# Performance work log

Hardware: AMD Instinct MI355X
Metric: run time of the kernel (lower is better)

The kernel has to match this reference:

```python
import jax, jax.numpy as jnp
import numpy as np
import math

B, S, D, H, PD = 2, 2048, 1024, 16, 3
DK = D // H          # 64
SP = S // H          # 128, required so physics_scores matches scores shape


def setup_inputs() -> dict:
    key = jax.random.key(0)
    ks = jax.random.split(key, 16)
    sc = 0.02
    return {
        "query": jax.random.normal(ks[0], (B, S, D), jnp.float32),
        "key_in": jax.random.normal(ks[1], (B, S, D), jnp.float32),
        "value": jax.random.normal(ks[2], (B, S, D), jnp.float32),
        "physics_info": jax.random.normal(ks[3], (B, SP, PD), jnp.float32),
        "Wq": jax.random.normal(ks[4], (D, D), jnp.float32) * sc,
        "bq": jnp.zeros((D,), jnp.float32),
        "Wk": jax.random.normal(ks[5], (D, D), jnp.float32) * sc,
        "bk": jnp.zeros((D,), jnp.float32),
        "Wv": jax.random.normal(ks[6], (D, D), jnp.float32) * sc,
        "bv": jnp.zeros((D,), jnp.float32),
        "Wo": jax.random.normal(ks[7], (D, D), jnp.float32) * sc,
        "bo": jnp.zeros((D,), jnp.float32),
        "Pw": jax.random.normal(ks[8], (PD, D), jnp.float32),   # physics_weight
        "pb": jnp.zeros((1,), jnp.float32),                      # physics_bias
    }


def reference(query, key_in, value, physics_info, Wq, bq, Wk, bk, Wv, bv, Wo, bo, Pw, pb):
    b, s, d = query.shape
    inv = 1.0 / math.sqrt(DK)
    # project and split heads -> [B, H, S, DK]
    Q = (query @ Wq + bq).reshape(b, s, H, DK).transpose(0, 2, 1, 3)
    K = (key_in @ Wk + bk).reshape(b, s, H, DK).transpose(0, 2, 1, 3)
    V = (value @ Wv + bv).reshape(b, s, H, DK).transpose(0, 2, 1, 3)
    scores = jnp.einsum('bhqd,bhkd->bhqk', Q, K) * inv  # [B,H,S,S]
    # physics constraint: [B,SP,D] -> (expand over heads is a no-op) -> [B,SP*H,DK]
    pc = (physics_info @ Pw).reshape(b, SP * H, DK)
    physics_scores = jnp.einsum('bhqd,bkd->bhqk', Q, pc) * inv  # [B,H,S,S]
    scores = scores + pb[0] * physics_scores
    attn = jax.nn.softmax(scores, axis=-1)  # dropout in eval mode (identity)
    ctx = jnp.einsum('bhqk,bhkd->bhqd', attn, V)
    ctx = ctx.transpose(0, 2, 1, 3).reshape(b, s, d)
    return ctx @ Wo + bo
```

## Files before the change

### kernel.cpp

```cpp
#include <hip/hip_runtime.h>
#include <hip/hip_bf16.h>
#include <stdint.h>
#include <math.h>

typedef __bf16 bf16_t;
typedef __attribute__((ext_vector_type(8))) __bf16 bf16x8;
typedef __attribute__((ext_vector_type(4))) __bf16 bf16x4;
typedef __attribute__((ext_vector_type(4))) short short4_t;
typedef __attribute__((ext_vector_type(4))) float f32x4;

#define GLOBAL_AS(p) ((const __attribute__((address_space(1))) void*)(p))
#define LDS_AS(p)    ((__attribute__((address_space(3))) void*)(p))

#define B_ 2
#define S_ 2048
#define D_ 1024
#define H_ 16
#define DK_ 64
#define SP_ 128

#define QSCALE 0.1803368801111144f

static __device__ inline float fast_exp2(float x) {
#if __has_builtin(__builtin_amdgcn_exp2f)
    return __builtin_amdgcn_exp2f(x);
#else
    return __expf(x * 0.6931471805599453f);
#endif
}

static __device__ inline f32x4 mfma16x16x16bf16(short4_t a, short4_t b, f32x4 c) {
#if __has_builtin(__builtin_amdgcn_mfma_f32_16x16x16bf16_1k)
    return __builtin_amdgcn_mfma_f32_16x16x16bf16_1k(a, b, c, 0, 0, 0);
#else
    asm volatile("v_mfma_f32_16x16x16_bf16 %0, %1, %2, %0" : "+v"(c) : "v"(a), "v"(b));
    return c;
#endif
}

struct WPtrs { const float* w[4]; bf16_t* o[4]; };

__global__ __launch_bounds__(256) void prep(
    const float* __restrict__ q, const float* __restrict__ k,
    const float* __restrict__ v,
    bf16_t* __restrict__ qo, bf16_t* __restrict__ ko, bf16_t* __restrict__ vo,
    WPtrs wp, const float* __restrict__ phys, const float* __restrict__ Pw,
    float* __restrict__ PP) {
    int bx = blockIdx.x, tid = threadIdx.x;
    if (bx < 6144) {
        int z = bx >> 11, blk = bx & 2047;
        const float* in = (z == 0) ? q : (z == 1) ? k : v;
        bf16_t* out = (z == 0) ? qo : (z == 1) ? ko : vo;
        size_t i = ((size_t)blk * 256 + tid) * 8;
        f32x4 a = *(const f32x4*)(in + i);
        f32x4 b = *(const f32x4*)(in + i + 4);
        bf16x8 o;
#pragma unroll
        for (int e = 0; e < 4; ++e) { o[e] = (bf16_t)a[e]; o[4 + e] = (bf16_t)b[e]; }
        *(bf16x8*)(out + i) = o;
    } else if (bx < 10240) {
        __shared__ bf16_t t[32][33];
        int idx = bx - 6144;
        int z = idx >> 10;
        const float* W = wp.w[z];
        bf16_t* Wt = wp.o[z];
        int gx = (idx & 31) * 32, gy = ((idx >> 5) & 31) * 32;
        int x = tid & 31, y0 = tid >> 5;
#pragma unroll
        for (int j = 0; j < 32; j += 8)
            t[y0 + j][x] = (bf16_t)W[(size_t)(gy + y0 + j) * D_ + gx + x];
        __syncthreads();
#pragma unroll
        for (int j = 0; j < 32; j += 8)
            Wt[(size_t)(gx + y0 + j) * D_ + gy + x] = t[x][y0 + j];
    } else {
        int i = (bx - 10240) * 256 + tid;
        int n = i & (D_ - 1);
        int sb = i >> 10;
        float acc = 0.f;
#pragma unroll
        for (int p = 0; p < 3; ++p)
            acc += phys[sb * 3 + p] * Pw[p * D_ + n];
        PP[i] = acc;
    }
}

#define TSTR 272

__global__ __launch_bounds__(256) void qkv_gemm(
    const bf16_t* __restrict__ Qi, const bf16_t* __restrict__ Ki,
    const bf16_t* __restrict__ Vi,
    const bf16_t* __restrict__ WqT, const bf16_t* __restrict__ WkT,
    const bf16_t* __restrict__ WvT,
    const float* __restrict__ bq, const float* __restrict__ bk,
    const float* __restrict__ bv,
    bf16_t* __restrict__ Qo, bf16_t* __restrict__ Ko, bf16_t* __restrict__ Vo,
    const float* __restrict__ PP, const float* __restrict__ pbp) {
    __shared__ alignas(16) char smem[40960];
    bf16_t* lA = (bf16_t*)smem;
    bf16_t* lB = (bf16_t*)(smem + 16384);
    int z = blockIdx.z;
    const bf16_t* A = (z == 0) ? Qi : (z == 1) ? Ki : Vi;
    const bf16_t* Bt = (z == 0) ? WqT : (z == 1) ? WkT : WvT;
    const float* bias = (z == 0) ? bq : (z == 1) ? bk : bv;

    int tid = threadIdx.x;
    int lane = tid & 63, wid = tid >> 6;
    int quad = lane >> 4, l15 = lane & 15;
    int bm = blockIdx.x * 128;
    int bn = blockIdx.y * 128;
    int wm = (wid >> 1) * 64, wn = (wid & 1) * 64;
    f32x4 acc[4][4] = {};

    for (int k0 = 0; k0 < D_; k0 += 64) {
        __syncthreads();
        const char* gA = (const char*)(A + (size_t)bm * D_ + k0);
        const char* gB = (const char*)(Bt + (size_t)bn * D_ + k0);
#pragma unroll
        for (int j = 0; j < 4; ++j) {
            int woff = j * 4096 + wid * 1024;
            int fl = woff + lane * 16;
            int row = fl >> 7, col = fl & 127;
            __builtin_amdgcn_global_load_lds(GLOBAL_AS(gA + (size_t)row * (D_ * 2) + col),
                                             LDS_AS((char*)lA + woff), 16, 0, 0);
            __builtin_amdgcn_global_load_lds(GLOBAL_AS(gB + (size_t)row * (D_ * 2) + col),
                                             LDS_AS((char*)lB + woff), 16, 0, 0);
        }
        __syncthreads();
#pragma unroll
        for (int ks = 0; ks < 2; ++ks) {
            bf16x8 af[4], bfr[4];
#pragma unroll
            for (int i = 0; i < 4; ++i) {
                af[i] = *(const bf16x8*)((const char*)lA + (wm + i * 16 + l15) * 128 + ks * 64 + quad * 16);
                bfr[i] = *(const bf16x8*)((const char*)lB + (wn + i * 16 + l15) * 128 + ks * 64 + quad * 16);
            }
#pragma unroll
            for (int i = 0; i < 4; ++i)
#pragma unroll
                for (int j = 0; j < 4; ++j)
                    acc[i][j] = __builtin_amdgcn_mfma_f32_16x16x32_bf16(af[i], bfr[j], acc[i][j], 0, 0, 0);
        }
    }

    __syncthreads();
    float pb0 = (z == 1) ? pbp[0] : 0.f;
    char* T = smem;
#pragma unroll
    for (int i = 0; i < 4; ++i)
#pragma unroll
        for (int j = 0; j < 4; ++j) {
            int rl0 = wm + i * 16 + quad * 4;
            int c = wn + j * 16 + l15;
            float bv_ = bias[bn + c];
            if (z == 2) {
                bf16x4 t4;
#pragma unroll
                for (int reg = 0; reg < 4; ++reg) t4[reg] = (bf16_t)(acc[i][j][reg] + bv_);
                *(bf16x4*)(T + c * TSTR + rl0 * 2) = t4;
            } else if (z == 1) {
#pragma unroll
                for (int reg = 0; reg < 4; ++reg) {
                    int r = bm + rl0 + reg;
                    int b = r >> 11, s = r & (S_ - 1);
                    float v = acc[i][j][reg] + bv_ +
                              pb0 * PP[((size_t)(b * SP_ + (s >> 4)) << 10) + ((s & 15) << 6) + ((bn + c) & 63)];
                    *(bf16_t*)(T + (rl0 + reg) * TSTR + c * 2) = (bf16_t)v;
                }
            } else {
#pragma unroll
                for (int reg = 0; reg < 4; ++reg)
                    *(bf16_t*)(T + (rl0 + reg) * TSTR + c * 2) = (bf16_t)((acc[i][j][reg] + bv_) * QSCALE);
            }
        }
    __syncthreads();
    if (z == 2) {
        int b = bm >> 11, s0 = bm & (S_ - 1);
        char* gout = (char*)Vo + (((size_t)(b << 10) + bn) * S_ + s0) * 2;
#pragma unroll
        for (int it = 0; it < 8; ++it) {
            int chunk = it * 256 + tid;
            int row = chunk >> 4, c16 = chunk & 15;
            bf16x8 v = *(const bf16x8*)(T + row * TSTR + c16 * 16);
            *(bf16x8*)(gout + (size_t)row * (S_ * 2) + c16 * 16) = v;
        }
    } else {
        bf16_t* O = (z == 0) ? Qo : Ko;
        char* gout = (char*)(O + (size_t)bm * D_ + bn);
#pragma unroll
        for (int it = 0; it < 8; ++it) {
            int chunk = it * 256 + tid;
            int row = chunk >> 4, c16 = chunk & 15;
            bf16x8 v = *(const bf16x8*)(T + row * TSTR + c16 * 16);
            *(bf16x8*)(gout + (size_t)row * (D_ * 2) + c16 * 16) = v;
        }
    }
}

#define KSTR 144
#define VSTR 272

__global__ __launch_bounds__(256) void flash_attn(const bf16_t* Qb,
                                                  const bf16_t* __restrict__ Kb,
                                                  const bf16_t* __restrict__ Vt,
                                                  bf16_t* Ctx) {
    __shared__ alignas(16) char lK[128 * KSTR];
    __shared__ alignas(16) char lV[64 * VSTR];
    int tid = threadIdx.x, lane = tid & 63, wid = tid >> 6;
    int quad = lane >> 4, l15 = lane & 15;
    int q0 = blockIdx.x * 128;
    int h = blockIdx.y, b = blockIdx.z;
    const bf16_t* Qh = Qb + ((size_t)b * S_) * D_ + h * DK_;
    const bf16_t* Kh = Kb + ((size_t)b * S_) * D_ + h * DK_;
    const bf16_t* Vh = Vt + ((size_t)b * D_ + h * DK_) * S_;

    {
        const char* g = (const char*)(Qh + (size_t)q0 * D_);
#pragma unroll
        for (int j = 0; j < 4; ++j) {
            int flat = j * 4096 + tid * 16;
            bf16x8 v = *(const bf16x8*)(g + (size_t)(flat >> 7) * (D_ * 2) + (flat & 127));
            *(bf16x8*)(lK + (flat >> 7) * KSTR + (flat & 127)) = v;
        }
    }
    __syncthreads();
    bf16x8 qf[2][2];
#pragma unroll
    for (int mt = 0; mt < 2; ++mt)
#pragma unroll
        for (int ks = 0; ks < 2; ++ks)
            qf[mt][ks] = *(const bf16x8*)(lK + (wid * 32 + mt * 16 + l15) * KSTR + ks * 64 + quad * 16);

    f32x4 ot[4][2] = {};
    float l_i[2] = {0.f, 0.f};

    for (int t = 0; t < S_ / 128; ++t) {
        const char* gK = (const char*)(Kh + (size_t)t * 128 * D_);
        const char* gV = (const char*)(Vh + (size_t)t * 128);
        bf16x8 vk[4], vv[4];
#pragma unroll
        for (int j = 0; j < 4; ++j) {
            int flat = j * 4096 + tid * 16;
            vk[j] = *(const bf16x8*)(gK + (size_t)(flat >> 7) * (D_ * 2) + (flat & 127));
            vv[j] = *(const bf16x8*)(gV + (size_t)(flat >> 8) * (S_ * 2) + (flat & 255));
        }
        __syncthreads();
#pragma unroll
        for (int j = 0; j < 4; ++j) {
            int flat = j * 4096 + tid * 16;
            *(bf16x8*)(lK + (flat >> 7) * KSTR + (flat & 127)) = vk[j];
            *(bf16x8*)(lV + (flat >> 8) * VSTR + (flat & 255)) = vv[j];
        }
        __syncthreads();

        f32x4 sc[8][2];
#pragma unroll
        for (int kt = 0; kt < 8; ++kt)
#pragma unroll
            for (int mt = 0; mt < 2; ++mt) sc[kt][mt] = (f32x4){0.f, 0.f, 0.f, 0.f};
#pragma unroll
        for (int kt = 0; kt < 8; ++kt) {
            bf16x8 kf0 = *(const bf16x8*)(lK + (kt * 16 + l15) * KSTR + quad * 16);
            bf16x8 kf1 = *(const bf16x8*)(lK + (kt * 16 + l15) * KSTR + 64 + quad * 16);
#pragma unroll
            for (int mt = 0; mt < 2; ++mt) {
                sc[kt][mt] = __builtin_amdgcn_mfma_f32_16x16x32_bf16(kf0, qf[mt][0], sc[kt][mt], 0, 0, 0);
                sc[kt][mt] = __builtin_amdgcn_mfma_f32_16x16x32_bf16(kf1, qf[mt][1], sc[kt][mt], 0, 0, 0);
            }
        }

#pragma unroll
        for (int mt = 0; mt < 2; ++mt) {
            float rsum = 0.f;
#pragma unroll
            for (int kt = 0; kt < 8; ++kt)
#pragma unroll
                for (int r = 0; r < 4; ++r) {
                    float p = fast_exp2(sc[kt][mt][r]);
                    sc[kt][mt][r] = p;
                    rsum += p;
                }
            rsum += __shfl_xor(rsum, 16, 64);
            rsum += __shfl_xor(rsum, 32, 64);
            l_i[mt] += rsum;
        }

#pragma unroll
        for (int kt = 0; kt < 8; ++kt) {
            short4_t bp[2];
#pragma unroll
            for (int mt = 0; mt < 2; ++mt) {
                bf16x4 t4;
#pragma unroll
                for (int r = 0; r < 4; ++r) t4[r] = (bf16_t)sc[kt][mt][r];
                bp[mt] = *(short4_t*)&t4;
            }
#pragma unroll
            for (int dt = 0; dt < 4; ++dt) {
                bf16x4 a4 = *(const bf16x4*)(lV + (dt * 16 + l15) * VSTR + kt * 32 + quad * 8);
                short4_t ap = *(short4_t*)&a4;
#pragma unroll
                for (int mt = 0; mt < 2; ++mt)
                    ot[dt][mt] = mfma16x16x16bf16(ap, bp[mt], ot[dt][mt]);
            }
        }
    }

    __syncthreads();
#pragma unroll
    for (int mt = 0; mt < 2; ++mt) {
        float inv_l = 1.0f / l_i[mt];
#pragma unroll
        for (int dt = 0; dt < 4; ++dt) {
            bf16x4 t4;
#pragma unroll
            for (int r = 0; r < 4; ++r) t4[r] = (bf16_t)(ot[dt][mt][r] * inv_l);
            *(bf16x4*)(lK + (wid * 32 + mt * 16 + l15) * KSTR + dt * 32 + quad * 8) = t4;
        }
    }
    __syncthreads();
    {
        char* gout = (char*)(Ctx + ((size_t)b * S_ + q0) * D_ + h * DK_);
#pragma unroll
        for (int j = 0; j < 4; ++j) {
            int flat = j * 4096 + tid * 16;
            bf16x8 v = *(const bf16x8*)(lK + (flat >> 7) * KSTR + (flat & 127));
            *(bf16x8*)(gout + (size_t)(flat >> 7) * (D_ * 2) + (flat & 127)) = v;
        }
    }
}

__global__ __launch_bounds__(256) void gemm_out(const bf16_t* __restrict__ A,
                                                const bf16_t* __restrict__ Bt,
                                                const float* __restrict__ bias,
                                                float* __restrict__ C) {
    __shared__ alignas(16) bf16_t lA[128 * 64];
    __shared__ alignas(16) bf16_t lB[128 * 64];
    int tid = threadIdx.x;
    int lane = tid & 63, wid = tid >> 6;
    int quad = lane >> 4, l15 = lane & 15;
    int bm = blockIdx.x * 128;
    int bn = blockIdx.y * 128;
    int wm = (wid >> 1) * 64, wn = (wid & 1) * 64;
    f32x4 acc[4][4] = {};

    for (int k0 = 0; k0 < D_; k0 += 64) {
        __syncthreads();
        const char* gA = (const char*)(A + (size_t)bm * D_ + k0);
        const char* gB = (const char*)(Bt + (size_t)bn * D_ + k0);
#pragma unroll
        for (int j = 0; j < 4; ++j) {
            int woff = j * 4096 + wid * 1024;
            int fl = woff + lane * 16;
            int row = fl >> 7, col = fl & 127;
            __builtin_amdgcn_global_load_lds(GLOBAL_AS(gA + (size_t)row * (D_ * 2) + col),
                                             LDS_AS((char*)lA + woff), 16, 0, 0);
            __builtin_amdgcn_global_load_lds(GLOBAL_AS(gB + (size_t)row * (D_ * 2) + col),
                                             LDS_AS((char*)lB + woff), 16, 0, 0);
        }
        __syncthreads();
#pragma unroll
        for (int ks = 0; ks < 2; ++ks) {
            bf16x8 af[4], bfr[4];
#pragma unroll
            for (int i = 0; i < 4; ++i) {
                af[i] = *(const bf16x8*)((const char*)lA + (wm + i * 16 + l15) * 128 + ks * 64 + quad * 16);
                bfr[i] = *(const bf16x8*)((const char*)lB + (wn + i * 16 + l15) * 128 + ks * 64 + quad * 16);
            }
#pragma unroll
            for (int i = 0; i < 4; ++i)
#pragma unroll
                for (int j = 0; j < 4; ++j)
                    acc[i][j] = __builtin_amdgcn_mfma_f32_16x16x32_bf16(af[i], bfr[j], acc[i][j], 0, 0, 0);
        }
    }
#pragma unroll
    for (int i = 0; i < 4; ++i)
#pragma unroll
        for (int j = 0; j < 4; ++j) {
            int r0 = bm + wm + i * 16 + quad * 4;
            int c = bn + wn + j * 16 + l15;
            float bv_ = bias[c];
#pragma unroll
            for (int reg = 0; reg < 4; ++reg)
                C[(size_t)(r0 + reg) * D_ + c] = acc[i][j][reg] + bv_;
        }
}

extern "C" void kernel_launch(void* const* d_in, const int* in_sizes, int n_in,
                              void* d_out, int out_size, void* d_ws, size_t ws_size,
                              hipStream_t stream) {
    const float* query  = (const float*)d_in[0];
    const float* key_in = (const float*)d_in[1];
    const float* value  = (const float*)d_in[2];
    const float* phys   = (const float*)d_in[3];
    const float* Wq     = (const float*)d_in[4];
    const float* bq     = (const float*)d_in[5];
    const float* Wk     = (const float*)d_in[6];
    const float* bk     = (const float*)d_in[7];
    const float* Wv     = (const float*)d_in[8];
    const float* bv     = (const float*)d_in[9];
    const float* Wo     = (const float*)d_in[10];
    const float* bo     = (const float*)d_in[11];
    const float* Pw     = (const float*)d_in[12];
    const float* pb     = (const float*)d_in[13];

    char* ws = (char*)d_ws;
    const size_t MB = 1ull << 20;
    bf16_t* Kb  = (bf16_t*)(ws + 0 * MB);
    bf16_t* QC  = (bf16_t*)(ws + 8 * MB);
    bf16_t* Kin = (bf16_t*)(ws + 16 * MB);
    bf16_t* Vin = (bf16_t*)(ws + 24 * MB);
    bf16_t* WqT = (bf16_t*)(ws + 32 * MB);
    bf16_t* WkT = (bf16_t*)(ws + 34 * MB);
    bf16_t* WvT = (bf16_t*)(ws + 36 * MB);
    bf16_t* WoT = (bf16_t*)(ws + 38 * MB);
    float*  PP  = (float*)(ws + 40 * MB);
    bf16_t* Vt  = (bf16_t*)d_out;
    bf16_t* Qin = (bf16_t*)((char*)d_out + 8 * MB);

    WPtrs wp;
    wp.w[0] = Wq; wp.w[1] = Wk; wp.w[2] = Wv; wp.w[3] = Wo;
    wp.o[0] = WqT; wp.o[1] = WkT; wp.o[2] = WvT; wp.o[3] = WoT;

    prep<<<11264, 256, 0, stream>>>(query, key_in, value, Qin, Kin, Vin,
                                    wp, phys, Pw, PP);

    dim3 gq(32, 8, 3);
    qkv_gemm<<<gq, 256, 0, stream>>>(Qin, Kin, Vin, WqT, WkT, WvT,
                                     bq, bk, bv, QC, Kb, Vt, PP, pb);

    dim3 fg(S_ / 128, H_, B_);
    flash_attn<<<fg, 256, 0, stream>>>(QC, Kb, Vt, QC);

    dim3 gg(32, 8);
    gemm_out<<<gg, 256, 0, stream>>>(QC, WoT, bo, (float*)d_out);
}
```

Baseline: 249.2 us.

## Double-buffer flash attention K/V via direct-to-LDS loads with XOR swizzle

Rewrites the attention kernel's K/V staging to use global_load_lds into double-buffered LDS tiles. The next tile's load is issued before computing on the current one, so memory latency overlaps MFMA work. Padded LDS strides are replaced with XOR-swizzled layouts to avoid bank conflicts. The grid is remapped to a 1D launch so heads sharing K/V land on the same XCD, and s_setprio is raised around the MFMA sections. The costs are 64KB of LDS per block, which lowers occupancy, and more complex manual waitcnt and barrier handling.

New measurement: 263.4 us. 5.7% more time.

```diff
diff --git a/kernel.cpp b/kernel.cpp
--- a/kernel.cpp
+++ b/kernel.cpp
@@ -197,19 +197,21 @@
     }
 }
 
-#define KSTR 144
-#define VSTR 272
-
 __global__ __launch_bounds__(256) void flash_attn(const bf16_t* Qb,
                                                   const bf16_t* __restrict__ Kb,
                                                   const bf16_t* __restrict__ Vt,
                                                   bf16_t* Ctx) {
-    __shared__ alignas(16) char lK[128 * KSTR];
-    __shared__ alignas(16) char lV[64 * VSTR];
+    __shared__ alignas(16) char lds[65536];
     int tid = threadIdx.x, lane = tid & 63, wid = tid >> 6;
     int quad = lane >> 4, l15 = lane & 15;
-    int q0 = blockIdx.x * 128;
-    int h = blockIdx.y, b = blockIdx.z;
+    int r7 = l15 & 7;
+
+    int bid = blockIdx.x;
+    int xcd = bid & 7, slot = bid >> 3;
+    int yz = xcd * 4 + (slot >> 4);
+    int q0 = (slot & 15) * 128;
+    int h = yz & 15, b = yz >> 4;
+
     const bf16_t* Qh = Qb + ((size_t)b * S_) * D_ + h * DK_;
     const bf16_t* Kh = Kb + ((size_t)b * S_) * D_ + h * DK_;
     const bf16_t* Vh = Vt + ((size_t)b * D_ + h * DK_) * S_;
@@ -219,8 +221,9 @@
 #pragma unroll
         for (int j = 0; j < 4; ++j) {
             int flat = j * 4096 + tid * 16;
-            bf16x8 v = *(const bf16x8*)(g + (size_t)(flat >> 7) * (D_ * 2) + (flat & 127));
-            *(bf16x8*)(lK + (flat >> 7) * KSTR + (flat & 127)) = v;
+            int row = flat >> 7, ch = (flat >> 4) & 7;
+            bf16x8 v = *(const bf16x8*)(g + (size_t)row * (D_ * 2) + (ch << 4));
+            *(bf16x8*)(lds + row * 128 + ((ch ^ (row & 7)) << 4)) = v;
         }
     }
     __syncthreads();
@@ -229,45 +232,69 @@
     for (int mt = 0; mt < 2; ++mt)
 #pragma unroll
         for (int ks = 0; ks < 2; ++ks)
-            qf[mt][ks] = *(const bf16x8*)(lK + (wid * 32 + mt * 16 + l15) * KSTR + ks * 64 + quad * 16);
+            qf[mt][ks] = *(const bf16x8*)(lds + (wid * 32 + mt * 16 + l15) * 128 +
+                                          ((((ks << 2) | quad) ^ r7) << 4));
+    asm volatile("s_waitcnt lgkmcnt(0)" ::: "memory");
+    __builtin_amdgcn_sched_barrier(0);
+    __builtin_amdgcn_s_barrier();
+
+    auto STAGE = [&](int t) {
+        char* bK = lds + (t & 1) * 16384;
+        char* bV = lds + 32768 + (t & 1) * 16384;
+        const char* gK = (const char*)(Kh + (size_t)t * 128 * D_);
+        const char* gV = (const char*)(Vh + (size_t)t * 128);
+#pragma unroll
+        for (int j = 0; j < 4; ++j) {
+            int flat = j * 4096 + tid * 16;
+            int row = flat >> 7, ch = (flat >> 4) & 7;
+            __builtin_amdgcn_global_load_lds(
+                GLOBAL_AS(gK + (size_t)row * (D_ * 2) + ((ch ^ (row & 7)) << 4)),
+                LDS_AS(bK + flat), 16, 0, 0);
+        }
+#pragma unroll
+        for (int j = 0; j < 4; ++j) {
+            int flat = j * 4096 + tid * 16;
+            int row = flat >> 8, ch = (flat >> 4) & 15;
+            __builtin_amdgcn_global_load_lds(
+                GLOBAL_AS(gV + (size_t)row * (S_ * 2) + ((ch ^ (row & 15)) << 4)),
+                LDS_AS(bV + flat), 16, 0, 0);
+        }
+    };
 
     f32x4 ot[4][2] = {};
     float l_i[2] = {0.f, 0.f};
 
+    STAGE(0);
+
     for (int t = 0; t < S_ / 128; ++t) {
-        const char* gK = (const char*)(Kh + (size_t)t * 128 * D_);
-        const char* gV = (const char*)(Vh + (size_t)t * 128);
-        bf16x8 vk[4], vv[4];
-#pragma unroll
-        for (int j = 0; j < 4; ++j) {
-            int flat = j * 4096 + tid * 16;
-            vk[j] = *(const bf16x8*)(gK + (size_t)(flat >> 7) * (D_ * 2) + (flat & 127));
-            vv[j] = *(const bf16x8*)(gV + (size_t)(flat >> 8) * (S_ * 2) + (flat & 255));
-        }
-        __syncthreads();
-#pragma unroll
-        for (int j = 0; j < 4; ++j) {
-            int flat = j * 4096 + tid * 16;
-            *(bf16x8*)(lK + (flat >> 7) * KSTR + (flat & 127)) = vk[j];
-            *(bf16x8*)(lV + (flat >> 8) * VSTR + (flat & 255)) = vv[j];
-        }
-        __syncthreads();
+        asm volatile("s_waitcnt vmcnt(0)" ::: "memory");
+        __builtin_amdgcn_s_barrier();
+        __builtin_amdgcn_sched_barrier(0);
+
+        if (t < S_ / 128 - 1) STAGE(t + 1);
+        __builtin_amdgcn_sched_barrier(0);
+
+        const char* bK = lds + (t & 1) * 16384;
+        const char* bV = lds + 32768 + (t & 1) * 16384;
 
         f32x4 sc[8][2];
 #pragma unroll
         for (int kt = 0; kt < 8; ++kt)
 #pragma unroll
             for (int mt = 0; mt < 2; ++mt) sc[kt][mt] = (f32x4){0.f, 0.f, 0.f, 0.f};
+        __builtin_amdgcn_s_setprio(1);
 #pragma unroll
         for (int kt = 0; kt < 8; ++kt) {
-            bf16x8 kf0 = *(const bf16x8*)(lK + (kt * 16 + l15) * KSTR + quad * 16);
-            bf16x8 kf1 = *(const bf16x8*)(lK + (kt * 16 + l15) * KSTR + 64 + quad * 16);
+            int row = kt * 16 + l15;
+            bf16x8 kf0 = *(const bf16x8*)(bK + row * 128 + ((quad ^ r7) << 4));
+            bf16x8 kf1 = *(const bf16x8*)(bK + row * 128 + (((quad | 4) ^ r7) << 4));
 #pragma unroll
             for (int mt = 0; mt < 2; ++mt) {
                 sc[kt][mt] = __builtin_amdgcn_mfma_f32_16x16x32_bf16(kf0, qf[mt][0], sc[kt][mt], 0, 0, 0);
                 sc[kt][mt] = __builtin_amdgcn_mfma_f32_16x16x32_bf16(kf1, qf[mt][1], sc[kt][mt], 0, 0, 0);
             }
         }
+        __builtin_amdgcn_s_setprio(0);
 
 #pragma unroll
         for (int mt = 0; mt < 2; ++mt) {
@@ -285,6 +312,7 @@
             l_i[mt] += rsum;
         }
 
+        __builtin_amdgcn_s_setprio(1);
 #pragma unroll
         for (int kt = 0; kt < 8; ++kt) {
             short4_t bp[2];
@@ -297,25 +325,30 @@
             }
 #pragma unroll
             for (int dt = 0; dt < 4; ++dt) {
-                bf16x4 a4 = *(const bf16x4*)(lV + (dt * 16 + l15) * VSTR + kt * 32 + quad * 8);
+                int row = dt * 16 + l15;
+                int ch = (kt * 2 + (quad >> 1)) ^ l15;
+                bf16x4 a4 = *(const bf16x4*)(bV + row * 256 + (ch << 4) + ((quad & 1) << 3));
                 short4_t ap = *(short4_t*)&a4;
 #pragma unroll
                 for (int mt = 0; mt < 2; ++mt)
                     ot[dt][mt] = mfma16x16x16bf16(ap, bp[mt], ot[dt][mt]);
             }
         }
+        __builtin_amdgcn_s_setprio(0);
     }
 
     __syncthreads();
 #pragma unroll
     for (int mt = 0; mt < 2; ++mt) {
         float inv_l = 1.0f / l_i[mt];
+        int row = wid * 32 + mt * 16 + l15;
 #pragma unroll
         for (int dt = 0; dt < 4; ++dt) {
             bf16x4 t4;
 #pragma unroll
             for (int r = 0; r < 4; ++r) t4[r] = (bf16_t)(ot[dt][mt][r] * inv_l);
-            *(bf16x4*)(lK + (wid * 32 + mt * 16 + l15) * KSTR + dt * 32 + quad * 8) = t4;
+            int ch = (dt * 2 + (quad >> 1)) ^ r7;
+            *(bf16x4*)(lds + row * 128 + (ch << 4) + ((quad & 1) << 3)) = t4;
         }
     }
     __syncthreads();
@@ -324,8 +357,9 @@
 #pragma unroll
         for (int j = 0; j < 4; ++j) {
             int flat = j * 4096 + tid * 16;
-            bf16x8 v = *(const bf16x8*)(lK + (flat >> 7) * KSTR + (flat & 127));
-            *(bf16x8*)(gout + (size_t)(flat >> 7) * (D_ * 2) + (flat & 127)) = v;
+            int row = flat >> 7, ch = (flat >> 4) & 7;
+            bf16x8 v = *(const bf16x8*)(lds + row * 128 + ((ch ^ (row & 7)) << 4));
+            *(bf16x8*)(gout + (size_t)row * (D_ * 2) + (ch << 4)) = v;
         }
     }
 }
@@ -430,8 +464,7 @@
     qkv_gemm<<<gq, 256, 0, stream>>>(Qin, Kin, Vin, WqT, WkT, WvT,
                                      bq, bk, bv, QC, Kb, Vt, PP, pb);
 
-    dim3 fg(S_ / 128, H_, B_);
-    flash_attn<<<fg, 256, 0, stream>>>(QC, Kb, Vt, QC);
+    flash_attn<<<512, 256, 0, stream>>>(QC, Kb, Vt, QC);
 
     dim3 gg(32, 8);
     gemm_out<<<gg, 256, 0, stream>>>(QC, WoT, bo, (float*)d_out);
```

## Restructure flash attention to 8 waves with prefetch, XCD-aware block mapping, setprio

Applied to the files above, without the earlier changes.

The flash attention kernel now runs 512 threads per block, so each wave owns 16 query rows instead of 32, which halves per-wave register state and allows more waves per CU. The next K/V tile is loaded into registers while the current tile is being computed, overlapping global loads with MFMA work. A 1D grid is remapped so that blocks landing on the same XCD share the same (batch, head) and reuse K/V in L2. s_setprio raises wave priority around the MFMA sections. The trade-offs are that each K/V tile in LDS is now amortized over fewer query rows per wave, and every block pays more barrier overhead.

Result: no change. 253.4 us (+1.7%).

```diff
diff --git a/kernel.cpp b/kernel.cpp
--- a/kernel.cpp
+++ b/kernel.cpp
@@ -200,16 +200,21 @@
 #define KSTR 144
 #define VSTR 272
 
-__global__ __launch_bounds__(256) void flash_attn(const bf16_t* Qb,
-                                                  const bf16_t* __restrict__ Kb,
-                                                  const bf16_t* __restrict__ Vt,
-                                                  bf16_t* Ctx) {
+__global__ __launch_bounds__(512, 4) void flash_attn(const bf16_t* Qb,
+                                                     const bf16_t* __restrict__ Kb,
+                                                     const bf16_t* __restrict__ Vt,
+                                                     bf16_t* Ctx) {
     __shared__ alignas(16) char lK[128 * KSTR];
     __shared__ alignas(16) char lV[64 * VSTR];
     int tid = threadIdx.x, lane = tid & 63, wid = tid >> 6;
     int quad = lane >> 4, l15 = lane & 15;
-    int q0 = blockIdx.x * 128;
-    int h = blockIdx.y, b = blockIdx.z;
+
+    int bid = blockIdx.x;
+    int xcd = bid & 7, slot = bid >> 3;
+    int yz = xcd * 4 + (slot >> 4);
+    int q0 = (slot & 15) * 128;
+    int h = yz & 15, b = yz >> 4;
+
     const bf16_t* Qh = Qb + ((size_t)b * S_) * D_ + h * DK_;
     const bf16_t* Kh = Kb + ((size_t)b * S_) * D_ + h * DK_;
     const bf16_t* Vh = Vt + ((size_t)b * D_ + h * DK_) * S_;
@@ -217,113 +222,113 @@
     {
         const char* g = (const char*)(Qh + (size_t)q0 * D_);
 #pragma unroll
-        for (int j = 0; j < 4; ++j) {
-            int flat = j * 4096 + tid * 16;
+        for (int j = 0; j < 2; ++j) {
+            int flat = j * 8192 + tid * 16;
             bf16x8 v = *(const bf16x8*)(g + (size_t)(flat >> 7) * (D_ * 2) + (flat & 127));
             *(bf16x8*)(lK + (flat >> 7) * KSTR + (flat & 127)) = v;
         }
     }
     __syncthreads();
-    bf16x8 qf[2][2];
-#pragma unroll
-    for (int mt = 0; mt < 2; ++mt)
-#pragma unroll
-        for (int ks = 0; ks < 2; ++ks)
-            qf[mt][ks] = *(const bf16x8*)(lK + (wid * 32 + mt * 16 + l15) * KSTR + ks * 64 + quad * 16);
-
-    f32x4 ot[4][2] = {};
-    float l_i[2] = {0.f, 0.f};
-
-    for (int t = 0; t < S_ / 128; ++t) {
-        const char* gK = (const char*)(Kh + (size_t)t * 128 * D_);
-        const char* gV = (const char*)(Vh + (size_t)t * 128);
-        bf16x8 vk[4], vv[4];
-#pragma unroll
-        for (int j = 0; j < 4; ++j) {
-            int flat = j * 4096 + tid * 16;
+    bf16x8 qf[2];
+#pragma unroll
+    for (int ks = 0; ks < 2; ++ks)
+        qf[ks] = *(const bf16x8*)(lK + (wid * 16 + l15) * KSTR + ks * 64 + quad * 16);
+    __syncthreads();
+
+    f32x4 ot[4] = {};
+    float l_i = 0.f;
+
+    bf16x8 vk[2], vv[2];
+    const int NT = S_ / 128;
+    {
+        const char* gK = (const char*)Kh;
+        const char* gV = (const char*)Vh;
+#pragma unroll
+        for (int j = 0; j < 2; ++j) {
+            int flat = j * 8192 + tid * 16;
             vk[j] = *(const bf16x8*)(gK + (size_t)(flat >> 7) * (D_ * 2) + (flat & 127));
             vv[j] = *(const bf16x8*)(gV + (size_t)(flat >> 8) * (S_ * 2) + (flat & 255));
         }
-        __syncthreads();
-#pragma unroll
-        for (int j = 0; j < 4; ++j) {
-            int flat = j * 4096 + tid * 16;
+    }
+
+    for (int t = 0; t < NT; ++t) {
+#pragma unroll
+        for (int j = 0; j < 2; ++j) {
+            int flat = j * 8192 + tid * 16;
             *(bf16x8*)(lK + (flat >> 7) * KSTR + (flat & 127)) = vk[j];
             *(bf16x8*)(lV + (flat >> 8) * VSTR + (flat & 255)) = vv[j];
         }
         __syncthreads();
 
-        f32x4 sc[8][2];
-#pragma unroll
-        for (int kt = 0; kt < 8; ++kt)
-#pragma unroll
-            for (int mt = 0; mt < 2; ++mt) sc[kt][mt] = (f32x4){0.f, 0.f, 0.f, 0.f};
+        if (t + 1 < NT) {
+            const char* gK = (const char*)(Kh + (size_t)(t + 1) * 128 * D_);
+            const char* gV = (const char*)(Vh + (size_t)(t + 1) * 128);
+#pragma unroll
+            for (int j = 0; j < 2; ++j) {
+                int flat = j * 8192 + tid * 16;
+                vk[j] = *(const bf16x8*)(gK + (size_t)(flat >> 7) * (D_ * 2) + (flat & 127));
+                vv[j] = *(const bf16x8*)(gV + (size_t)(flat >> 8) * (S_ * 2) + (flat & 255));
+            }
+        }
+
+        f32x4 sc[8];
+#pragma unroll
+        for (int kt = 0; kt < 8; ++kt) sc[kt] = (f32x4){0.f, 0.f, 0.f, 0.f};
+        __builtin_amdgcn_s_setprio(1);
 #pragma unroll
         for (int kt = 0; kt < 8; ++kt) {
             bf16x8 kf0 = *(const bf16x8*)(lK + (kt * 16 + l15) * KSTR + quad * 16);
             bf16x8 kf1 = *(const bf16x8*)(lK + (kt * 16 + l15) * KSTR + 64 + quad * 16);
-#pragma unroll
-            for (int mt = 0; mt < 2; ++mt) {
-                sc[kt][mt] = __builtin_amdgcn_mfma_f32_16x16x32_bf16(kf0, qf[mt][0], sc[kt][mt], 0, 0, 0);
-                sc[kt][mt] = __builtin_amdgcn_mfma_f32_16x16x32_bf16(kf1, qf[mt][1], sc[kt][mt], 0, 0, 0);
-            }
-        }
-
-#pragma unroll
-        for (int mt = 0; mt < 2; ++mt) {
-            float rsum = 0.f;
-#pragma unroll
-            for (int kt = 0; kt < 8; ++kt)
-#pragma unroll
-                for (int r = 0; r < 4; ++r) {
-                    float p = fast_exp2(sc[kt][mt][r]);
-                    sc[kt][mt][r] = p;
-                    rsum += p;
-                }
-            rsum += __shfl_xor(rsum, 16, 64);
-            rsum += __shfl_xor(rsum, 32, 64);
-            l_i[mt] += rsum;
-        }
-
+            sc[kt] = __builtin_amdgcn_mfma_f32_16x16x32_bf16(kf0, qf[0], sc[kt], 0, 0, 0);
+            sc[kt] = __builtin_amdgcn_mfma_f32_16x16x32_bf16(kf1, qf[1], sc[kt], 0, 0, 0);
+        }
+        __builtin_amdgcn_s_setprio(0);
+
+        float rsum = 0.f;
+#pragma unroll
+        for (int kt = 0; kt < 8; ++kt)
+#pragma unroll
+            for (int r = 0; r < 4; ++r) {
+                float p = fast_exp2(sc[kt][r]);
+                sc[kt][r] = p;
+                rsum += p;
+            }
+        rsum += __shfl_xor(rsum, 16, 64);
+        rsum += __shfl_xor(rsum, 32, 64);
+        l_i += rsum;
+
+        __builtin_amdgcn_s_setprio(1);
 #pragma unroll
         for (int kt = 0; kt < 8; ++kt) {
-            short4_t bp[2];
-#pragma unroll
-            for (int mt = 0; mt < 2; ++mt) {
-                bf16x4 t4;
-#pragma unroll
-                for (int r = 0; r < 4; ++r) t4[r] = (bf16_t)sc[kt][mt][r];
-                bp[mt] = *(short4_t*)&t4;
-            }
+            bf16x4 t4;
+#pragma unroll
+            for (int r = 0; r < 4; ++r) t4[r] = (bf16_t)sc[kt][r];
+            short4_t bp = *(short4_t*)&t4;
 #pragma unroll
             for (int dt = 0; dt < 4; ++dt) {
                 bf16x4 a4 = *(const bf16x4*)(lV + (dt * 16 + l15) * VSTR + kt * 32 + quad * 8);
                 short4_t ap = *(short4_t*)&a4;
-#pragma unroll
-                for (int mt = 0; mt < 2; ++mt)
-                    ot[dt][mt] = mfma16x16x16bf16(ap, bp[mt], ot[dt][mt]);
-            }
-        }
-    }
-
-    __syncthreads();
-#pragma unroll
-    for (int mt = 0; mt < 2; ++mt) {
-        float inv_l = 1.0f / l_i[mt];
-#pragma unroll
-        for (int dt = 0; dt < 4; ++dt) {
-            bf16x4 t4;
-#pragma unroll
-            for (int r = 0; r < 4; ++r) t4[r] = (bf16_t)(ot[dt][mt][r] * inv_l);
-            *(bf16x4*)(lK + (wid * 32 + mt * 16 + l15) * KSTR + dt * 32 + quad * 8) = t4;
-        }
+                ot[dt] = mfma16x16x16bf16(ap, bp, ot[dt]);
+            }
+        }
+        __builtin_amdgcn_s_setprio(0);
+        __syncthreads();
+    }
+
+    float inv_l = 1.0f / l_i;
+#pragma unroll
+    for (int dt = 0; dt < 4; ++dt) {
+        bf16x4 t4;
+#pragma unroll
+        for (int r = 0; r < 4; ++r) t4[r] = (bf16_t)(ot[dt][r] * inv_l);
+        *(bf16x4*)(lK + (wid * 16 + l15) * KSTR + dt * 32 + quad * 8) = t4;
     }
     __syncthreads();
     {
         char* gout = (char*)(Ctx + ((size_t)b * S_ + q0) * D_ + h * DK_);
 #pragma unroll
-        for (int j = 0; j < 4; ++j) {
-            int flat = j * 4096 + tid * 16;
+        for (int j = 0; j < 2; ++j) {
+            int flat = j * 8192 + tid * 16;
             bf16x8 v = *(const bf16x8*)(lK + (flat >> 7) * KSTR + (flat & 127));
             *(bf16x8*)(gout + (size_t)(flat >> 7) * (D_ * 2) + (flat & 127)) = v;
         }
@@ -430,8 +435,7 @@
     qkv_gemm<<<gq, 256, 0, stream>>>(Qin, Kin, Vin, WqT, WkT, WvT,
                                      bq, bk, bv, QC, Kb, Vt, PP, pb);
 
-    dim3 fg(S_ / 128, H_, B_);
-    flash_attn<<<fg, 256, 0, stream>>>(QC, Kb, Vt, QC);
+    flash_attn<<<512, 512, 0, stream>>>(QC, Kb, Vt, QC);
 
     dim3 gg(32, 8);
     gemm_out<<<gg, 256, 0, stream>>>(QC, WoT, bo, (float*)d_out);
```

## Prefetch 256-key K/V tiles into registers, remap blocks per XCD, add setprio

Applied to the files above, without the earlier changes.

The attention loop now stages 256 keys per iteration and issues the global loads for the next tile before computing on the current one, so memory latency overlaps with MFMA work and there are fewer barriers. Blocks are launched on a 1D grid and remapped so that each XCD handles a contiguous set of (batch, head) pairs, which is meant to improve L2 reuse of K/V. MFMA sections are wrapped in s_setprio to favour matrix issue. The cost is higher register use (16 prefetch vectors) and roughly double the LDS, which may reduce occupancy.

Measured after the change: 260.3 us. +4.4%, slower.

```diff
diff --git a/kernel.cpp b/kernel.cpp
--- a/kernel.cpp
+++ b/kernel.cpp
@@ -198,18 +198,23 @@
 }
 
 #define KSTR 144
-#define VSTR 272
+#define VSTR2 528
 
 __global__ __launch_bounds__(256) void flash_attn(const bf16_t* Qb,
                                                   const bf16_t* __restrict__ Kb,
                                                   const bf16_t* __restrict__ Vt,
                                                   bf16_t* Ctx) {
-    __shared__ alignas(16) char lK[128 * KSTR];
-    __shared__ alignas(16) char lV[64 * VSTR];
+    __shared__ alignas(16) char lK[256 * KSTR];
+    __shared__ alignas(16) char lV[64 * VSTR2];
     int tid = threadIdx.x, lane = tid & 63, wid = tid >> 6;
     int quad = lane >> 4, l15 = lane & 15;
-    int q0 = blockIdx.x * 128;
-    int h = blockIdx.y, b = blockIdx.z;
+
+    int bid = blockIdx.x;
+    int xcd = bid & 7, slot = bid >> 3;
+    int yz = xcd * 4 + (slot >> 4);
+    int q0 = (slot & 15) * 128;
+    int h = yz & 15, b = yz >> 4;
+
     const bf16_t* Qh = Qb + ((size_t)b * S_) * D_ + h * DK_;
     const bf16_t* Kh = Kb + ((size_t)b * S_) * D_ + h * DK_;
     const bf16_t* Vh = Vt + ((size_t)b * D_ + h * DK_) * S_;
@@ -230,83 +235,107 @@
 #pragma unroll
         for (int ks = 0; ks < 2; ++ks)
             qf[mt][ks] = *(const bf16x8*)(lK + (wid * 32 + mt * 16 + l15) * KSTR + ks * 64 + quad * 16);
+    __syncthreads();
 
     f32x4 ot[4][2] = {};
     float l_i[2] = {0.f, 0.f};
 
-    for (int t = 0; t < S_ / 128; ++t) {
-        const char* gK = (const char*)(Kh + (size_t)t * 128 * D_);
-        const char* gV = (const char*)(Vh + (size_t)t * 128);
-        bf16x8 vk[4], vv[4];
-#pragma unroll
-        for (int j = 0; j < 4; ++j) {
-            int flat = j * 4096 + tid * 16;
-            vk[j] = *(const bf16x8*)(gK + (size_t)(flat >> 7) * (D_ * 2) + (flat & 127));
-            vv[j] = *(const bf16x8*)(gV + (size_t)(flat >> 8) * (S_ * 2) + (flat & 255));
-        }
-        __syncthreads();
-#pragma unroll
-        for (int j = 0; j < 4; ++j) {
-            int flat = j * 4096 + tid * 16;
-            *(bf16x8*)(lK + (flat >> 7) * KSTR + (flat & 127)) = vk[j];
-            *(bf16x8*)(lV + (flat >> 8) * VSTR + (flat & 255)) = vv[j];
-        }
-        __syncthreads();
-
-        f32x4 sc[8][2];
-#pragma unroll
-        for (int kt = 0; kt < 8; ++kt)
-#pragma unroll
-            for (int mt = 0; mt < 2; ++mt) sc[kt][mt] = (f32x4){0.f, 0.f, 0.f, 0.f};
-#pragma unroll
-        for (int kt = 0; kt < 8; ++kt) {
-            bf16x8 kf0 = *(const bf16x8*)(lK + (kt * 16 + l15) * KSTR + quad * 16);
-            bf16x8 kf1 = *(const bf16x8*)(lK + (kt * 16 + l15) * KSTR + 64 + quad * 16);
+    bf16x8 vk[8], vv[8];
+    const int NP = S_ / 256;
+    {
+        const char* gK = (const char*)Kh;
+        const char* gV = (const char*)Vh;
+#pragma unroll
+        for (int j = 0; j < 8; ++j) {
+            int fk = j * 4096 + tid * 16;
+            vk[j] = *(const bf16x8*)(gK + (size_t)(fk >> 7) * (D_ * 2) + (fk & 127));
+            vv[j] = *(const bf16x8*)(gV + (size_t)(fk >> 9) * (S_ * 2) + (fk & 511));
+        }
+    }
+
+    for (int t = 0; t < NP; ++t) {
+#pragma unroll
+        for (int j = 0; j < 8; ++j) {
+            int fk = j * 4096 + tid * 16;
+            *(bf16x8*)(lK + (fk >> 7) * KSTR + (fk & 127)) = vk[j];
+            *(bf16x8*)(lV + (fk >> 9) * VSTR2 + (fk & 511)) = vv[j];
+        }
+        __syncthreads();
+
+        if (t + 1 < NP) {
+            const char* gK = (const char*)(Kh + (size_t)(t + 1) * 256 * D_);
+            const char* gV = (const char*)(Vh + (size_t)(t + 1) * 256);
+#pragma unroll
+            for (int j = 0; j < 8; ++j) {
+                int fk = j * 4096 + tid * 16;
+                vk[j] = *(const bf16x8*)(gK + (size_t)(fk >> 7) * (D_ * 2) + (fk & 127));
+                vv[j] = *(const bf16x8*)(gV + (size_t)(fk >> 9) * (S_ * 2) + (fk & 511));
+            }
+        }
+
+#pragma unroll
+        for (int kk = 0; kk < 2; ++kk) {
+            f32x4 sc[8][2];
+#pragma unroll
+            for (int kt = 0; kt < 8; ++kt)
+#pragma unroll
+                for (int mt = 0; mt < 2; ++mt) sc[kt][mt] = (f32x4){0.f, 0.f, 0.f, 0.f};
+            __builtin_amdgcn_s_setprio(1);
+#pragma unroll
+            for (int kt = 0; kt < 8; ++kt) {
+                int row = kk * 128 + kt * 16 + l15;
+                bf16x8 kf0 = *(const bf16x8*)(lK + row * KSTR + quad * 16);
+                bf16x8 kf1 = *(const bf16x8*)(lK + row * KSTR + 64 + quad * 16);
+#pragma unroll
+                for (int mt = 0; mt < 2; ++mt) {
+                    sc[kt][mt] = __builtin_amdgcn_mfma_f32_16x16x32_bf16(kf0, qf[mt][0], sc[kt][mt], 0, 0, 0);
+                    sc[kt][mt] = __builtin_amdgcn_mfma_f32_16x16x32_bf16(kf1, qf[mt][1], sc[kt][mt], 0, 0, 0);
+                }
+            }
+            __builtin_amdgcn_s_setprio(0);
+
 #pragma unroll
             for (int mt = 0; mt < 2; ++mt) {
-                sc[kt][mt] = __builtin_amdgcn_mfma_f32_16x16x32_bf16(kf0, qf[mt][0], sc[kt][mt], 0, 0, 0);
-                sc[kt][mt] = __builtin_amdgcn_mfma_f32_16x16x32_bf16(kf1, qf[mt][1], sc[kt][mt], 0, 0, 0);
-            }
-        }
-
-#pragma unroll
-        for (int mt = 0; mt < 2; ++mt) {
-            float rsum = 0.f;
-#pragma unroll
-            for (int kt = 0; kt < 8; ++kt)
-#pragma unroll
-                for (int r = 0; r < 4; ++r) {
-                    float p = fast_exp2(sc[kt][mt][r]);
-                    sc[kt][mt][r] = p;
-                    rsum += p;
+                float rsum = 0.f;
+#pragma unroll
+                for (int kt = 0; kt < 8; ++kt)
+#pragma unroll
+                    for (int r = 0; r < 4; ++r) {
+                        float p = fast_exp2(sc[kt][mt][r]);
+                        sc[kt][mt][r] = p;
+                        rsum += p;
+                    }
+                rsum += __shfl_xor(rsum, 16, 64);
+                rsum += __shfl_xor(rsum, 32, 64);
+                l_i[mt] += rsum;
+            }
+
+            __builtin_amdgcn_s_setprio(1);
+#pragma unroll
+            for (int kt = 0; kt < 8; ++kt) {
+                short4_t bp[2];
+#pragma unroll
+                for (int mt = 0; mt < 2; ++mt) {
+                    bf16x4 t4;
+#pragma unroll
+                    for (int r = 0; r < 4; ++r) t4[r] = (bf16_t)sc[kt][mt][r];
+                    bp[mt] = *(short4_t*)&t4;
                 }
-            rsum += __shfl_xor(rsum, 16, 64);
-            rsum += __shfl_xor(rsum, 32, 64);
-            l_i[mt] += rsum;
-        }
-
-#pragma unroll
-        for (int kt = 0; kt < 8; ++kt) {
-            short4_t bp[2];
-#pragma unroll
-            for (int mt = 0; mt < 2; ++mt) {
-                bf16x4 t4;
-#pragma unroll
-                for (int r = 0; r < 4; ++r) t4[r] = (bf16_t)sc[kt][mt][r];
-                bp[mt] = *(short4_t*)&t4;
-            }
-#pragma unroll
-            for (int dt = 0; dt < 4; ++dt) {
-                bf16x4 a4 = *(const bf16x4*)(lV + (dt * 16 + l15) * VSTR + kt * 32 + quad * 8);
-                short4_t ap = *(short4_t*)&a4;
-#pragma unroll
-                for (int mt = 0; mt < 2; ++mt)
-                    ot[dt][mt] = mfma16x16x16bf16(ap, bp[mt], ot[dt][mt]);
-            }
-        }
-    }
-
-    __syncthreads();
+#pragma unroll
+                for (int dt = 0; dt < 4; ++dt) {
+                    bf16x4 a4 = *(const bf16x4*)(lV + (dt * 16 + l15) * VSTR2 +
+                                                 kk * 256 + kt * 32 + quad * 8);
+                    short4_t ap = *(short4_t*)&a4;
+#pragma unroll
+                    for (int mt = 0; mt < 2; ++mt)
+                        ot[dt][mt] = mfma16x16x16bf16(ap, bp[mt], ot[dt][mt]);
+                }
+            }
+            __builtin_amdgcn_s_setprio(0);
+        }
+        __syncthreads();
+    }
+
 #pragma unroll
     for (int mt = 0; mt < 2; ++mt) {
         float inv_l = 1.0f / l_i[mt];
@@ -430,8 +459,7 @@
     qkv_gemm<<<gq, 256, 0, stream>>>(Qin, Kin, Vin, WqT, WkT, WvT,
                                      bq, bk, bv, QC, Kb, Vt, PP, pb);
 
-    dim3 fg(S_ / 128, H_, B_);
-    flash_attn<<<fg, 256, 0, stream>>>(QC, Kb, Vt, QC);
+    flash_attn<<<512, 256, 0, stream>>>(QC, Kb, Vt, QC);
 
     dim3 gg(32, 8);
     gemm_out<<<gg, 256, 0, stream>>>(QC, WoT, bo, (float*)d_out);
```
